# Performance work log

Hardware: AMD Instinct MI355X
Metric: run time of the kernel (lower is better)

## Reference

```python
import jax, jax.numpy as jnp
import numpy as np
from jax import lax

NUM_CLASSES = 102
IN_CAPS = 2592
IN_DIM = 8
OUT_DIM = 16
ROUTINGS = 3
IMG = 112

def squash(s, axis=-1, eps=1e-8):
    sq = jnp.sum(s * s, axis=axis, keepdims=True)
    return (sq / (1.0 + sq)) * s / jnp.sqrt(sq + eps)

def conv2d(x, w, b, stride):
    y = lax.conv_general_dilated(x, w, (stride, stride), 'VALID',
                                 dimension_numbers=('NCHW', 'OIHW', 'NCHW'))
    return y + b[None, :, None, None]

def setup_inputs() -> dict:
    key = jax.random.key(0)
    ks = jax.random.split(key, 12)
    B = 32
    x = jax.random.normal(ks[0], (B, 3, IMG, IMG), jnp.float32)
    targets = jax.random.randint(ks[1], (B,), 0, NUM_CLASSES)
    conv1_w = jax.random.normal(ks[2], (256, 3, 11, 11), jnp.float32) * 0.02
    conv1_b = jnp.zeros((256,), jnp.float32)
    pc_w = jax.random.normal(ks[3], (256, 256, 9, 9), jnp.float32) * 0.02
    pc_b = jnp.zeros((256,), jnp.float32)
    W = jax.random.normal(ks[4], (NUM_CLASSES, IN_CAPS, OUT_DIM, IN_DIM), jnp.float32) * 0.01
    fc1_w = jax.random.normal(ks[5], (NUM_CLASSES * OUT_DIM, 512), jnp.float32) * 0.02
    fc1_b = jnp.zeros((512,), jnp.float32)
    fc2_w = jax.random.normal(ks[6], (512, 1024), jnp.float32) * 0.02
    fc2_b = jnp.zeros((1024,), jnp.float32)
    fc3_w = jax.random.normal(ks[7], (1024, 3 * IMG * IMG), jnp.float32) * 0.02
    fc3_b = jnp.zeros((3 * IMG * IMG,), jnp.float32)
    return dict(x=x, targets=targets, conv1_w=conv1_w, conv1_b=conv1_b,
                pc_w=pc_w, pc_b=pc_b, W=W,
                fc1_w=fc1_w, fc1_b=fc1_b, fc2_w=fc2_w, fc2_b=fc2_b,
                fc3_w=fc3_w, fc3_b=fc3_b)

def reference(x, targets, conv1_w, conv1_b, pc_w, pc_b, W,
              fc1_w, fc1_b, fc2_w, fc2_b, fc3_w, fc3_b):
    B = x.shape[0]
    # conv backbone: [B,3,112,112] -> [B,256,34,34]
    feat = jax.nn.relu(conv2d(x, conv1_w, conv1_b, 3))
    # primary caps conv: -> [B,256,9,9] -> [B,2592,8], squash
    pc = conv2d(feat, pc_w, pc_b, 3)
    u = squash(pc.reshape(B, IN_CAPS, IN_DIM))
    # prediction vectors: [B, O, N, D_out]
    x_hat = jnp.einsum('ondi,bni->bond', W, u)
    x_hat_sg = lax.stop_gradient(x_hat)
    b = jnp.zeros((B, NUM_CLASSES, IN_CAPS), x.dtype)
    v = None
    for it in range(ROUTINGS):
        c = jax.nn.softmax(b, axis=1)  # couple over out caps
        xh = x_hat if it == ROUTINGS - 1 else x_hat_sg
        s = jnp.einsum('bon,bond->bod', c, xh)
        v = squash(s)
        if it < ROUTINGS - 1:
            b = b + jnp.einsum('bond,bod->bon', xh, v)
    # reconstruction: mask by target class capsule
    mask = jax.nn.one_hot(targets, NUM_CLASSES, dtype=v.dtype)
    h = (v * mask[:, :, None]).reshape(B, NUM_CLASSES * OUT_DIM)
    h = jax.nn.relu(h @ fc1_w + fc1_b)
    h = jax.nn.relu(h @ fc2_w + fc2_b)
    recon = jax.nn.sigmoid(h @ fc3_w + fc3_b).reshape(B, 3, IMG, IMG)
    return (v, recon)
```

## Files before the change

### kernel.cpp

```cpp
#include <hip/hip_runtime.h>
#include <hip/hip_fp16.h>
#include <math.h>

#define B32   32
#define OCLS  102
#define NCAPS 2592

#define OFF_FEAT   0u
#define OFF_WQ2    0u
#define OFF_C1WT   10027008u
#define OFF_PCWQ   10119936u
#define OFF_PCP    15428352u
#define OFF_WQ     15428352u
#define OFF_U2     26045184u
#define OFF_CT     26708736u
#define OFF_FC3P   26045184u
#define OFF_S      30938880u
#define OFF_V0     30991104u
#define OFF_V1     31043328u
#define OFF_VSQ    31095552u
#define OFF_H1     31108608u
#define OFF_H2T    31124992u

typedef __attribute__((ext_vector_type(8))) short short8;
typedef __attribute__((ext_vector_type(4))) float f32x4;
typedef long long i64;

__device__ __forceinline__ unsigned short f2b(float f) {
  union { float f; unsigned u; } v; v.f = f;
  unsigned r = v.u + 0x7fffu + ((v.u >> 16) & 1u);
  return (unsigned short)(r >> 16);
}

__device__ __forceinline__ unsigned f2q_fast(float x) {
  union { float f; unsigned u; } v; v.f = x;
  unsigned s = (v.u >> 24) & 0x80u;
  unsigned au = v.u & 0x7fffffffu;
  if (au < 0x3c800000u) return s;
  if (au >= 0x43e00000u) return s | 0x7eu;
  unsigned r = au + 0x7ffffu + ((au >> 20) & 1u);
  unsigned e = (r >> 23) - 120u;
  unsigned m = (r >> 20) & 7u;
  return s | (e << 3) | m;
}

__device__ __forceinline__ unsigned fp8pair(float a, float b) {
#if __has_builtin(__builtin_amdgcn_cvt_pk_fp8_f32)
  return (unsigned)__builtin_amdgcn_cvt_pk_fp8_f32(a, b, 0, false) & 0xffffu;
#else
  return f2q_fast(a) | (f2q_fast(b) << 8);
#endif
}

__global__ void k_mkC1B(const float* __restrict__ conv1_w,
                        unsigned short* __restrict__ C1WB) {
  int co = blockIdx.x;
  int t = threadIdx.x;
#pragma unroll
  for (int ci = 0; ci < 3; ++ci) {
    float v = (t < 121) ? conv1_w[co * 363 + ci * 121 + t] : 0.f;
    C1WB[(ci * 256 + co) * 128 + t] = f2b(v);
  }
}

__global__ void k_mkBq(const float* __restrict__ pc_w, unsigned char* __restrict__ PCWQ) {
  int co = blockIdx.x;
  for (int e = threadIdx.x; e < 20736; e += 256) {
    int ci = e / 81, tap = e - ci * 81;
    PCWQ[(size_t)ci * 26624 + co * 104 + tap] =
        (unsigned char)f2q_fast(pc_w[(size_t)co * 20736 + e] * 64.f);
  }
  int ci = threadIdx.x;
  for (int tap = 81; tap < 104; ++tap)
    PCWQ[(size_t)ci * 26624 + co * 104 + tap] = 0;
}

__global__ __launch_bounds__(256) void k_mkW2(const float* __restrict__ W,
                                              unsigned char* __restrict__ Wq2,
                                              unsigned char* __restrict__ Wq) {
  __shared__ unsigned char sq[32 * 128];
  int t = threadIdx.x;
  size_t base = (size_t)blockIdx.x * 4096;
  const float4* src = (const float4*)(W + base + (size_t)t * 16);
  float4 f0 = src[0], f1 = src[1], f2 = src[2], f3 = src[3];
  float v[16] = {f0.x, f0.y, f0.z, f0.w, f1.x, f1.y, f1.z, f1.w,
                 f2.x, f2.y, f2.z, f2.w, f3.x, f3.y, f3.z, f3.w};
  unsigned words[4];
#pragma unroll
  for (int j = 0; j < 4; ++j)
    words[j] = fp8pair(v[4 * j] * 64.f, v[4 * j + 1] * 64.f) |
               (fp8pair(v[4 * j + 2] * 64.f, v[4 * j + 3] * 64.f) << 16);
  *(uint4*)(Wq2 + base + (size_t)t * 16) =
      make_uint4(words[0], words[1], words[2], words[3]);

  int r = t >> 3, seg = t & 7;
#pragma unroll
  for (int e = 0; e < 16; ++e) {
    unsigned byte = (words[e >> 2] >> ((e & 3) * 8)) & 0xffu;
    int idx = seg * 16 + e, d = idx >> 3, i = idx & 7;
    sq[r * 128 + i * 16 + d] = (unsigned char)byte;
  }
  __syncthreads();
  *(uint4*)(Wq + base + (size_t)t * 16) = ((const uint4*)sq)[t];
}

__global__ __launch_bounds__(256) void k_c1m(const float* __restrict__ x,
                                             const unsigned short* __restrict__ C1WB,
                                             const float* __restrict__ bias,
                                             float* __restrict__ feat2) {
  __shared__ unsigned short sh[48 * 128 + 128 * 128];
  unsigned short* lA = sh;
  unsigned short* lB = sh + 48 * 128;
  float* obuf = (float*)(sh + 48 * 128);

  int bx = blockIdx.x;
  int hf = blockIdx.y;
  int b = bx / 34, ho = bx % 34;
  int t = threadIdx.x;
  int lane = t & 63, wv = t >> 6;
  int l15 = lane & 15, lh = lane >> 4;
  int rx = l15 & 7;

  {
    uint4 zz = make_uint4(0, 0, 0, 0);
    uint4* z = (uint4*)lA;
    for (int i = t; i < 48 * 128 / 8; i += 256) z[i] = zz;
  }
  __syncthreads();

  f32x4 acc[3][2];
#pragma unroll
  for (int mf = 0; mf < 3; ++mf)
#pragma unroll
    for (int nf = 0; nf < 2; ++nf) acc[mf][nf] = (f32x4){0.f, 0.f, 0.f, 0.f};

#pragma unroll 1
  for (int ci = 0; ci < 3; ++ci) {
    {
      const uint4* Bsrc = (const uint4*)(C1WB + ci * 32768 + hf * 16384);
#pragma unroll
      for (int i = 0; i < 8; ++i) {
        int f = i * 256 + t;
        int row = f >> 4, cu = f & 15;
        ((uint4*)lB)[row * 16 + (cu ^ (row & 7))] = Bsrc[f];
      }
    }
    for (int tk = t; tk < 374; tk += 256) {
      int kh = tk / 34, wo = tk - kh * 34;
      const float* src = x + ((size_t)(b * 3 + ci) * 112 + ho * 3 + kh) * 112 + wo * 3;
#pragma unroll
      for (int j = 0; j < 11; ++j) {
        int tap = kh * 11 + j;
        int cu = tap >> 3;
        lA[wo * 128 + (((cu ^ (wo & 7)) << 3) | (tap & 7))] = f2b(src[j]);
      }
    }
    __syncthreads();

#pragma unroll
    for (int s = 0; s < 4; ++s) {
      int cub = ((s * 4 + lh) ^ rx) << 3;
      short8 a0 = *(const short8*)(lA + (0 + l15) * 128 + cub);
      short8 a1 = *(const short8*)(lA + (16 + l15) * 128 + cub);
      short8 a2 = *(const short8*)(lA + (32 + l15) * 128 + cub);
      short8 b0 = *(const short8*)(lB + (wv * 32 + 0 + l15) * 128 + cub);
      short8 b1 = *(const short8*)(lB + (wv * 32 + 16 + l15) * 128 + cub);
      acc[0][0] = __builtin_amdgcn_mfma_f32_16x16x32_bf16(a0, b0, acc[0][0], 0, 0, 0);
      acc[0][1] = __builtin_amdgcn_mfma_f32_16x16x32_bf16(a0, b1, acc[0][1], 0, 0, 0);
      acc[1][0] = __builtin_amdgcn_mfma_f32_16x16x32_bf16(a1, b0, acc[1][0], 0, 0, 0);
      acc[1][1] = __builtin_amdgcn_mfma_f32_16x16x32_bf16(a1, b1, acc[1][1], 0, 0, 0);
      acc[2][0] = __builtin_amdgcn_mfma_f32_16x16x32_bf16(a2, b0, acc[2][0], 0, 0, 0);
      acc[2][1] = __builtin_amdgcn_mfma_f32_16x16x32_bf16(a2, b1, acc[2][1], 0, 0, 0);
    }
    __syncthreads();
  }

  float bv[2];
#pragma unroll
  for (int nf = 0; nf < 2; ++nf) bv[nf] = bias[hf * 128 + wv * 32 + nf * 16 + l15];
#pragma unroll
  for (int mf = 0; mf < 3; ++mf)
#pragma unroll
    for (int nf = 0; nf < 2; ++nf)
#pragma unroll
      for (int r = 0; r < 4; ++r) {
        int wo = mf * 16 + lh * 4 + r;
        if (wo < 36)
          obuf[(wv * 32 + nf * 16 + l15) * 36 + wo] = fmaxf(acc[mf][nf][r] + bv[nf], 0.f);
      }
  __syncthreads();
  float4* dst = (float4*)(feat2 + (size_t)bx * 9216 + hf * 4608);
  const float4* srcb = (const float4*)obuf;
  for (int i = t; i < 1152; i += 256) dst[i] = srcb[i];
}

__device__ __forceinline__ void pc_gather8(const float* __restrict__ feat2,
                                           unsigned char* __restrict__ dstbuf,
                                           int mb, int ci, int t) {
  for (int task = t; task < 576; task += 256) {
    int m = task / 9, kh = task - m * 9;
    int gm = mb * 64 + m;
    if (gm < 2592) {
      int b = gm / 81, p = gm - b * 81;
      int ho = p / 9, wo = p - ho * 9;
      const float* src = feat2 + ((size_t)(b * 34 + ho * 3 + kh) * 256 + ci) * 36 + wo * 3;
      unsigned char* dst = dstbuf + m * 104 + kh * 9;
      unsigned p01 = fp8pair(src[0], src[1]);
      unsigned p23 = fp8pair(src[2], src[3]);
      unsigned p45 = fp8pair(src[4], src[5]);
      unsigned p67 = fp8pair(src[6], src[7]);
      unsigned p8  = fp8pair(src[8], 0.f);
      dst[0] = p01; dst[1] = p01 >> 8;
      dst[2] = p23; dst[3] = p23 >> 8;
      dst[4] = p45; dst[5] = p45 >> 8;
      dst[6] = p67; dst[7] = p67 >> 8;
      dst[8] = p8;
    }
  }
}

__global__ __launch_bounds__(256, 3) void k_pc4(const float* __restrict__ feat2,
                                                const unsigned char* __restrict__ PCWQ,
                                                __half* __restrict__ pcp) {
  __shared__ unsigned char lA[2][64 * 104];

  int mb = blockIdx.x, kc = blockIdx.y;
  int t = threadIdx.x;
  int lane = t & 63, wv = t >> 6;
  int l15 = lane & 15, lh = lane >> 4;

  {
    uint4 zz = make_uint4(0, 0, 0, 0);
    uint4* z = (uint4*)lA;
    for (int i = t; i < 2 * 64 * 104 / 16; i += 256) z[i] = zz;
  }
  __syncthreads();
  pc_gather8(feat2, lA[0], mb, kc * 8, t);
  __syncthreads();

  f32x4 acc[4][4];
#pragma unroll
  for (int mf = 0; mf < 4; ++mf)
#pragma unroll
    for (int nf = 0; nf < 4; ++nf) acc[mf][nf] = (f32x4){0.f, 0.f, 0.f, 0.f};

#pragma unroll 1
  for (int cil = 0; cil < 8; ++cil) {
    int ci = kc * 8 + cil;
    int cur = cil & 1;

    i64 bfr[4][3];
    const unsigned char* Bbase = PCWQ + (size_t)ci * 26624 + (wv * 64 + l15) * 104 + lh * 8;
#pragma unroll
    for (int nf = 0; nf < 4; ++nf)
#pragma unroll
      for (int s = 0; s < 3; ++s)
        bfr[nf][s] = *(const i64*)(Bbase + nf * 16 * 104 + s * 32);

    if (cil < 7) pc_gather8(feat2, lA[cur ^ 1], mb, ci + 1, t);

    const unsigned char* arow = lA[cur] + l15 * 104 + lh * 8;
#pragma unroll
    for (int s = 0; s < 3; ++s) {
      i64 a0 = *(const i64*)(arow + s * 32);
      i64 a1 = *(const i64*)(arow + 16 * 104 + s * 32);
      i64 a2 = *(const i64*)(arow + 32 * 104 + s * 32);
      i64 a3 = *(const i64*)(arow + 48 * 104 + s * 32);
      acc[0][0] = __builtin_amdgcn_mfma_f32_16x16x32_fp8_fp8(a0, bfr[0][s], acc[0][0], 0, 0, 0);
      acc[0][1] = __builtin_amdgcn_mfma_f32_16x16x32_fp8_fp8(a0, bfr[1][s], acc[0][1], 0, 0, 0);
      acc[0][2] = __builtin_amdgcn_mfma_f32_16x16x32_fp8_fp8(a0, bfr[2][s], acc[0][2], 0, 0, 0);
      acc[0][3] = __builtin_amdgcn_mfma_f32_16x16x32_fp8_fp8(a0, bfr[3][s], acc[0][3], 0, 0, 0);
      acc[1][0] = __builtin_amdgcn_mfma_f32_16x16x32_fp8_fp8(a1, bfr[0][s], acc[1][0], 0, 0, 0);
      acc[1][1] = __builtin_amdgcn_mfma_f32_16x16x32_fp8_fp8(a1, bfr[1][s], acc[1][1], 0, 0, 0);
      acc[1][2] = __builtin_amdgcn_mfma_f32_16x16x32_fp8_fp8(a1, bfr[2][s], acc[1][2], 0, 0, 0);
      acc[1][3] = __builtin_amdgcn_mfma_f32_16x16x32_fp8_fp8(a1, bfr[3][s], acc[1][3], 0, 0, 0);
      acc[2][0] = __builtin_amdgcn_mfma_f32_16x16x32_fp8_fp8(a2, bfr[0][s], acc[2][0], 0, 0, 0);
      acc[2][1] = __builtin_amdgcn_mfma_f32_16x16x32_fp8_fp8(a2, bfr[1][s], acc[2][1], 0, 0, 0);
      acc[2][2] = __builtin_amdgcn_mfma_f32_16x16x32_fp8_fp8(a2, bfr[2][s], acc[2][2], 0, 0, 0);
      acc[2][3] = __builtin_amdgcn_mfma_f32_16x16x32_fp8_fp8(a2, bfr[3][s], acc[2][3], 0, 0, 0);
      acc[3][0] = __builtin_amdgcn_mfma_f32_16x16x32_fp8_fp8(a3, bfr[0][s], acc[3][0], 0, 0, 0);
      acc[3][1] = __builtin_amdgcn_mfma_f32_16x16x32_fp8_fp8(a3, bfr[1][s], acc[3][1], 0, 0, 0);
      acc[3][2] = __builtin_amdgcn_mfma_f32_16x16x32_fp8_fp8(a3, bfr[2][s], acc[3][2], 0, 0, 0);
      acc[3][3] = __builtin_amdgcn_mfma_f32_16x16x32_fp8_fp8(a3, bfr[3][s], acc[3][3], 0, 0, 0);
    }
    __syncthreads();
  }

#pragma unroll
  for (int mf = 0; mf < 4; ++mf) {
    int gm = mb * 64 + mf * 16 + lh * 4;
    if (gm < 2592) {
      __half* dst = pcp + (size_t)kc * 663552 + (size_t)gm * 256 + wv * 64 + l15;
#pragma unroll
      for (int nf = 0; nf < 4; ++nf)
#pragma unroll
        for (int r = 0; r < 4; ++r)
          dst[(size_t)r * 256 + nf * 16] = __float2half(acc[mf][nf][r]);
    }
  }
}

__global__ __launch_bounds__(256) void k_rs(const __half* __restrict__ pcp,
                                            const float* __restrict__ pcb,
                                            float* __restrict__ u2) {
  __shared__ float tile[81 * 17];
  int b = blockIdx.x;
  int cog = blockIdx.y;
  int c0 = cog * 16;
  int t = threadIdx.x;

  for (int e = t; e < 1296; e += 256) {
    int p = e >> 4, col = e & 15;
    const __half* base = pcp + (size_t)(b * 81 + p) * 256 + c0 + col;
    float s = 0.f;
#pragma unroll
    for (int c = 0; c < 32; ++c) s += __half2float(base[(size_t)c * 663552]);
    tile[p * 17 + col] = pcb[c0 + col] + s * 0.015625f;
  }
  __syncthreads();

  if (t < 162) {
    float v[8];
    float sq = 0.f;
#pragma unroll
    for (int i = 0; i < 8; ++i) {
      int g = t * 8 + i;
      int col = g / 81, p = g - col * 81;
      v[i] = tile[p * 17 + col];
      sq += v[i] * v[i];
    }
    float sc = (sq / (1.f + sq)) / sqrtf(sq + 1e-8f);
    int n = cog * 162 + t;
    float4* dst = (float4*)(u2 + ((size_t)b * 2592 + n) * 8);
    dst[0] = make_float4(v[0] * sc, v[1] * sc, v[2] * sc, v[3] * sc);
    dst[1] = make_float4(v[4] * sc, v[5] * sc, v[6] * sc, v[7] * sc);
  }
}

__global__ __launch_bounds__(128) void k_A2(const unsigned char* __restrict__ Wq,
                                            const float* __restrict__ u2,
                                            const unsigned char* __restrict__ vq,
                                            __half* __restrict__ cT) {
  __shared__ __half Eld[102 * 2 * 2 * 32];
  int nb = blockIdx.x;
  int t = threadIdx.x, wv = t >> 6, lane = t & 63;
  int l15 = lane & 15, g = lane >> 4;
  int n0 = nb * 4 + 2 * wv;
  int nl = g >> 1, ih = (g & 1) * 4;

  float4 u0 = *(const float4*)(u2 + (((size_t)l15 * 2592 + n0 + nl) * 8 + ih));
  float4 u1 = *(const float4*)(u2 + (((size_t)(l15 + 16) * 2592 + n0 + nl) * 8 + ih));

  int nlA = l15 >> 3, iA = l15 & 7;
  const unsigned char* Ap = Wq + (((size_t)(n0 + nlA)) * 8 + iA) * 16 + (g & 1) * 8;
  const unsigned char* B0p = vq + (size_t)l15 * 16 + (g & 1) * 8;
  bool act = (g < 2);

  float den0 = 0.f, den1 = 0.f;
#pragma unroll 2
  for (int o = 0; o < 102; ++o) {
    i64 a = 0, b0 = 0, b1 = 0;
    if (act) {
      a  = *(const i64*)(Ap + (size_t)o * 331776);
      b0 = *(const i64*)(B0p + (size_t)o * 512);
      b1 = *(const i64*)(B0p + (size_t)o * 512 + 256);
    }
    f32x4 d0 = {0.f, 0.f, 0.f, 0.f}, d1 = {0.f, 0.f, 0.f, 0.f};
    d0 = __builtin_amdgcn_mfma_f32_16x16x32_fp8_fp8(a, b0, d0, 0, 0, 0);
    d1 = __builtin_amdgcn_mfma_f32_16x16x32_fp8_fp8(a, b1, d1, 0, 0, 0);
    float p0 = d0[0] * u0.x + d0[1] * u0.y + d0[2] * u0.z + d0[3] * u0.w;
    float p1 = d1[0] * u1.x + d1[1] * u1.y + d1[2] * u1.z + d1[3] * u1.w;
    p0 += __shfl_xor(p0, 16);
    p1 += __shfl_xor(p1, 16);
    p0 *= 1.52587890625e-05f;
    p1 *= 1.52587890625e-05f;
    float e0 = __expf(p0), e1 = __expf(p1);
    den0 += e0; den1 += e1;
    if ((g & 1) == 0) {
      int base = (o * 2 + wv) * 64 + (g >> 1) * 16 + l15;
      Eld[base] = __float2half(e0);
      Eld[base + 32] = __float2half(e1);
    }
  }
  float r0 = 1.0f / den0, r1 = 1.0f / den1;
  if ((g & 1) == 0) {
    for (int o = 0; o < 102; ++o) {
      int base = (o * 2 + wv) * 64 + (g >> 1) * 16 + l15;
      float c0 = __half2float(Eld[base]) * r0;
      float c1 = __half2float(Eld[base + 32]) * r1;
      __half* dst = cT + ((size_t)o * 2592 + n0 + (g >> 1)) * 32 + l15;
      dst[0] = __float2half(c0);
      dst[16] = __float2half(c1);
    }
  }
}

__device__ __forceinline__ i64 cu_pack8(float c, float4 a, float4 b) {
  union { unsigned u[2]; i64 v; } r;
  r.u[0] = fp8pair(c * a.x, c * a.y) | (fp8pair(c * a.z, c * a.w) << 16);
  r.u[1] = fp8pair(c * b.x, c * b.y) | (fp8pair(c * b.z, c * b.w) << 16);
  return r.v;
}

template <bool HASC>
__global__ __launch_bounds__(256) void k_B3(const unsigned char* __restrict__ Wq2,
                                            const float* __restrict__ u2,
                                            const __half* __restrict__ cT,
                                            float* __restrict__ s) {
  int o = blockIdx.x, kc = blockIdx.y;
  int t = threadIdx.x, lane = t & 63, wv = t >> 6;
  int l15 = lane & 15, h = lane >> 4;

  f32x4 acc0 = {0.f, 0.f, 0.f, 0.f}, acc1 = {0.f, 0.f, 0.f, 0.f};

#pragma unroll 1
  for (int st = wv; st < 54; st += 4) {
    int n = kc * 216 + st * 4 + h;
    i64 aq = *(const i64*)(Wq2 + (((size_t)o * 2592 + n) * 16 + l15) * 8);

    const float4* u0p = (const float4*)(u2 + ((size_t)l15 * 2592 + n) * 8);
    float4 u0a = u0p[0], u0b = u0p[1];
    const float4* u1p = (const float4*)(u2 + ((size_t)(l15 + 16) * 2592 + n) * 8);
    float4 u1a = u1p[0], u1b = u1p[1];

    float c0 = 16.0f, c1 = 16.0f;
    if (HASC) {
      const __half* cp = cT + ((size_t)o * 2592 + n) * 32;
      c0 = 16.0f * __half2float(cp[l15]);
      c1 = 16.0f * __half2float(cp[l15 + 16]);
    }
    i64 b0 = cu_pack8(c0, u0a, u0b);
    i64 b1 = cu_pack8(c1, u1a, u1b);

    acc0 = __builtin_amdgcn_mfma_f32_16x16x32_fp8_fp8(aq, b0, acc0, 0, 0, 0);
    acc1 = __builtin_amdgcn_mfma_f32_16x16x32_fp8_fp8(aq, b1, acc1, 0, 0, 0);
  }

#pragma unroll
  for (int r = 0; r < 4; ++r) {
    atomicAdd(s + ((size_t)l15 * 102 + o) * 16 + h * 4 + r, acc0[r]);
    atomicAdd(s + ((size_t)(l15 + 16) * 102 + o) * 16 + h * 4 + r, acc1[r]);
  }
}

__global__ void k_R(const float* __restrict__ s, float scale,
                    float* __restrict__ vout, const float* __restrict__ addin,
                    unsigned char* __restrict__ vsq, float* __restrict__ szero) {
  int t = blockIdx.x * 256 + threadIdx.x;
  if (t >= 3264) return;
  const float* sp = s + t * 16;
  float r[16];
  float sq = 0.f;
#pragma unroll
  for (int d = 0; d < 16; ++d) {
    r[d] = sp[d] * scale;
    sq += r[d] * r[d];
  }
  if (szero) {
#pragma unroll
    for (int d = 0; d < 16; ++d) szero[t * 16 + d] = 0.f;
  }
  float sc = (sq / (1.f + sq)) / sqrtf(sq + 1e-8f);
  float vv[16];
#pragma unroll
  for (int d = 0; d < 16; ++d) {
    vv[d] = r[d] * sc;
    vout[t * 16 + d] = vv[d];
  }
  if (vsq) {
    int b = t / 102, o = t - b * 102;
    float w[16];
#pragma unroll
    for (int d = 0; d < 16; ++d)
      w[d] = (addin ? (addin[t * 16 + d] + vv[d]) : vv[d]) * 1024.f;
    unsigned words[4];
#pragma unroll
    for (int q = 0; q < 4; ++q)
      words[q] = fp8pair(w[4 * q], w[4 * q + 1]) | (fp8pair(w[4 * q + 2], w[4 * q + 3]) << 16);
    *(uint4*)(vsq + ((size_t)o * 32 + b) * 16) =
        make_uint4(words[0], words[1], words[2], words[3]);
  }
}

__global__ void k_fc1(const float* __restrict__ v2, const int* __restrict__ tgt,
                      const float* __restrict__ w1, const float* __restrict__ b1,
                      float* __restrict__ h1) {
  int j = blockIdx.x * 128 + threadIdx.x;
  int bq = blockIdx.y;
#pragma unroll
  for (int bi = 0; bi < 4; ++bi) {
    int b = bq * 4 + bi;
    int tb = tgt[b];
    float acc = b1[j];
    const float* vv = v2 + (b * 102 + tb) * 16;
    const float* wr = w1 + (tb * 16) * 512 + j;
#pragma unroll
    for (int d = 0; d < 16; ++d) acc += vv[d] * wr[d * 512];
    h1[b * 512 + j] = fmaxf(acc, 0.f);
  }
}

__global__ void k_fc2(const float* __restrict__ h1, const float* __restrict__ w2,
                      const float* __restrict__ b2, float* __restrict__ h2T) {
  int j = blockIdx.x * 128 + threadIdx.x;
  int bq = blockIdx.y;
  float acc[4];
#pragma unroll
  for (int bi = 0; bi < 4; ++bi) acc[bi] = b2[j];
  for (int k = 0; k < 512; ++k) {
    float wv = w2[k * 1024 + j];
#pragma unroll
    for (int bi = 0; bi < 4; ++bi) acc[bi] += h1[(bq * 4 + bi) * 512 + k] * wv;
  }
  float4 o;
  o.x = fmaxf(acc[0], 0.f); o.y = fmaxf(acc[1], 0.f);
  o.z = fmaxf(acc[2], 0.f); o.w = fmaxf(acc[3], 0.f);
  *(float4*)(h2T + j * 32 + bq * 4) = o;
}

__global__ void k_fc3a(const float* __restrict__ h2T, const float* __restrict__ w3,
                       float* __restrict__ p) {
  int j = blockIdx.x * 128 + threadIdx.x;
  int ky = blockIdx.y;
  float acc[32];
#pragma unroll
  for (int i = 0; i < 32; ++i) acc[i] = 0.f;
  int k0 = ky * 256;
  for (int k = k0; k < k0 + 256; ++k) {
    float wv = w3[(size_t)k * 37632 + j];
    const float4* hp = (const float4*)(h2T + k * 32);
#pragma unroll
    for (int q = 0; q < 8; ++q) {
      float4 h = hp[q];
      acc[q * 4 + 0] += h.x * wv; acc[q * 4 + 1] += h.y * wv;
      acc[q * 4 + 2] += h.z * wv; acc[q * 4 + 3] += h.w * wv;
    }
  }
#pragma unroll
  for (int i = 0; i < 32; ++i)
    p[((size_t)ky * 32 + i) * 37632 + j] = acc[i];
}

__global__ void k_fc3b(const float* __restrict__ p, const float* __restrict__ b3,
                       float* __restrict__ out) {
  int j = blockIdx.x * 256 + threadIdx.x;
  float bv = b3[j];
#pragma unroll 1
  for (int b = 0; b < 32; ++b) {
    float s = bv + p[(size_t)b * 37632 + j] + p[(size_t)(32 + b) * 37632 + j] +
              p[(size_t)(64 + b) * 37632 + j] + p[(size_t)(96 + b) * 37632 + j];
    out[52224 + (size_t)b * 37632 + j] = 1.0f / (1.0f + __expf(-s));
  }
}

extern "C" void kernel_launch(void* const* d_in, const int* in_sizes, int n_in,
                              void* d_out, int out_size, void* d_ws, size_t ws_size,
                              hipStream_t stream) {
  const float* x       = (const float*)d_in[0];
  const int*   targets = (const int*)d_in[1];
  const float* conv1_w = (const float*)d_in[2];
  const float* conv1_b = (const float*)d_in[3];
  const float* pc_w    = (const float*)d_in[4];
  const float* pc_b    = (const float*)d_in[5];
  const float* W       = (const float*)d_in[6];
  const float* fc1_w   = (const float*)d_in[7];
  const float* fc1_b   = (const float*)d_in[8];
  const float* fc2_w   = (const float*)d_in[9];
  const float* fc2_b   = (const float*)d_in[10];
  const float* fc3_w   = (const float*)d_in[11];
  const float* fc3_b   = (const float*)d_in[12];
  float* out = (float*)d_out;
  float* ws = (float*)d_ws;

  float* FEAT2 = ws + OFF_FEAT;
  unsigned short* C1WB = (unsigned short*)(ws + OFF_C1WT);
  unsigned char* PCWQ = (unsigned char*)(ws + OFF_PCWQ);
  __half* PCP = (__half*)(ws + OFF_PCP);
  float* U2   = ws + OFF_U2;
  unsigned char* WQ2 = (unsigned char*)(ws + OFF_WQ2);
  unsigned char* WQ  = (unsigned char*)(ws + OFF_WQ);
  __half* CT  = (__half*)(ws + OFF_CT);
  float* FC3P = ws + OFF_FC3P;
  float* S    = ws + OFF_S;
  float* V0   = ws + OFF_V0;
  float* V1   = ws + OFF_V1;
  unsigned char* VSQ = (unsigned char*)(ws + OFF_VSQ);
  float* H1   = ws + OFF_H1;
  float* H2T  = ws + OFF_H2T;

  k_mkC1B<<<dim3(256), 128, 0, stream>>>(conv1_w, C1WB);
  k_mkBq<<<dim3(256), 256, 0, stream>>>(pc_w, PCWQ);

  k_c1m<<<dim3(1088, 2), 256, 0, stream>>>(x, C1WB, conv1_b, FEAT2);

  k_pc4<<<dim3(41, 32), 256, 0, stream>>>(FEAT2, PCWQ, PCP);
  k_rs<<<dim3(32, 16), 256, 0, stream>>>(PCP, pc_b, U2);

  k_mkW2<<<dim3(8262), 256, 0, stream>>>(W, WQ2, WQ);

  hipMemsetAsync(S, 0, 52224 * sizeof(float), stream);
  k_B3<false><<<dim3(102, 12), 256, 0, stream>>>(WQ2, U2, nullptr, S);
  k_R<<<dim3(13), 256, 0, stream>>>(S, 1.0f / (102.0f * 1024.0f), V0, nullptr, VSQ, S);

  k_A2<<<dim3(648), 128, 0, stream>>>(WQ, U2, VSQ, CT);
  k_B3<true><<<dim3(102, 12), 256, 0, stream>>>(WQ2, U2, CT, S);
  k_R<<<dim3(13), 256, 0, stream>>>(S, 1.0f / 1024.0f, V1, V0, VSQ, S);

  k_A2<<<dim3(648), 128, 0, stream>>>(WQ, U2, VSQ, CT);
  k_B3<true><<<dim3(102, 12), 256, 0, stream>>>(WQ2, U2, CT, S);
  k_R<<<dim3(13), 256, 0, stream>>>(S, 1.0f / 1024.0f, out, nullptr, nullptr, nullptr);

  k_fc1<<<dim3(4, 8), 128, 0, stream>>>(out, targets, fc1_w, fc1_b, H1);
  k_fc2<<<dim3(8, 8), 128, 0, stream>>>(H1, fc2_w, fc2_b, H2T);
  k_fc3a<<<dim3(294, 4), 128, 0, stream>>>(H2T, fc3_w, FC3P);
  k_fc3b<<<dim3(147), 256, 0, stream>>>(FC3P, fc3_b, out);
}
```

Before: 636.0 us.

## Merge weight-packing kernels, halve pc split-K, split softmax kernel over class chunks

Three packing kernels become one launch, and the workspace is re-laid out so the buffers no longer alias. The primary-caps conv split-K drops from 32 to 16 chunks, so the reduction kernel reads half as many partials while each block does twice the work. The coupling kernel is split three ways over output classes and writes unnormalised exponentials straight to global memory. It accumulates the softmax denominators atomically, and k_B3 now divides by them, with k_R zeroing the denominator buffer. This trades fewer launches and more parallelism in the routing step for extra atomics and extra global reads.

```diff
diff --git a/kernel.cpp b/kernel.cpp
--- a/kernel.cpp
+++ b/kernel.cpp
@@ -7,20 +7,21 @@
 #define NCAPS 2592
 
 #define OFF_FEAT   0u
-#define OFF_WQ2    0u
 #define OFF_C1WT   10027008u
-#define OFF_PCWQ   10119936u
-#define OFF_PCP    15428352u
-#define OFF_WQ     15428352u
-#define OFF_U2     26045184u
-#define OFF_CT     26708736u
-#define OFF_FC3P   26045184u
-#define OFF_S      30938880u
-#define OFF_V0     30991104u
-#define OFF_V1     31043328u
-#define OFF_VSQ    31095552u
-#define OFF_H1     31108608u
-#define OFF_H2T    31124992u
+#define OFF_PCWQ   10076160u
+#define OFF_PCP    11780096u
+#define OFF_WQ2    17088512u
+#define OFF_WQ     25555456u
+#define OFF_U2     34022400u
+#define OFF_CT     34685952u
+#define OFF_DEN    38916096u
+#define OFF_S      38999040u
+#define OFF_V0     39051264u
+#define OFF_V1     39103488u
+#define OFF_VSQ    39155712u
+#define OFF_H1     39168768u
+#define OFF_H2T    39185152u
+#define OFF_FC3P   39217920u
 
 typedef __attribute__((ext_vector_type(8))) short short8;
 typedef __attribute__((ext_vector_type(4))) float f32x4;
@@ -52,56 +53,64 @@
 #endif
 }
 
-__global__ void k_mkC1B(const float* __restrict__ conv1_w,
-                        unsigned short* __restrict__ C1WB) {
-  int co = blockIdx.x;
-  int t = threadIdx.x;
-#pragma unroll
-  for (int ci = 0; ci < 3; ++ci) {
-    float v = (t < 121) ? conv1_w[co * 363 + ci * 121 + t] : 0.f;
-    C1WB[(ci * 256 + co) * 128 + t] = f2b(v);
-  }
-}
-
-__global__ void k_mkBq(const float* __restrict__ pc_w, unsigned char* __restrict__ PCWQ) {
-  int co = blockIdx.x;
-  for (int e = threadIdx.x; e < 20736; e += 256) {
-    int ci = e / 81, tap = e - ci * 81;
-    PCWQ[(size_t)ci * 26624 + co * 104 + tap] =
-        (unsigned char)f2q_fast(pc_w[(size_t)co * 20736 + e] * 64.f);
-  }
-  int ci = threadIdx.x;
-  for (int tap = 81; tap < 104; ++tap)
-    PCWQ[(size_t)ci * 26624 + co * 104 + tap] = 0;
-}
-
-__global__ __launch_bounds__(256) void k_mkW2(const float* __restrict__ W,
+__device__ __forceinline__ float rcpf(float x) {
+#if __has_builtin(__builtin_amdgcn_rcpf)
+  return __builtin_amdgcn_rcpf(x);
+#else
+  return 1.0f / x;
+#endif
+}
+
+__global__ __launch_bounds__(256) void k_pack(const float* __restrict__ conv1_w,
+                                              const float* __restrict__ pc_w,
+                                              const float* __restrict__ W,
+                                              unsigned short* __restrict__ C1WB,
+                                              unsigned char* __restrict__ PCWQ,
                                               unsigned char* __restrict__ Wq2,
                                               unsigned char* __restrict__ Wq) {
   __shared__ unsigned char sq[32 * 128];
+  int bb = blockIdx.x;
   int t = threadIdx.x;
-  size_t base = (size_t)blockIdx.x * 4096;
-  const float4* src = (const float4*)(W + base + (size_t)t * 16);
-  float4 f0 = src[0], f1 = src[1], f2 = src[2], f3 = src[3];
-  float v[16] = {f0.x, f0.y, f0.z, f0.w, f1.x, f1.y, f1.z, f1.w,
-                 f2.x, f2.y, f2.z, f2.w, f3.x, f3.y, f3.z, f3.w};
-  unsigned words[4];
-#pragma unroll
-  for (int j = 0; j < 4; ++j)
-    words[j] = fp8pair(v[4 * j] * 64.f, v[4 * j + 1] * 64.f) |
-               (fp8pair(v[4 * j + 2] * 64.f, v[4 * j + 3] * 64.f) << 16);
-  *(uint4*)(Wq2 + base + (size_t)t * 16) =
-      make_uint4(words[0], words[1], words[2], words[3]);
-
-  int r = t >> 3, seg = t & 7;
-#pragma unroll
-  for (int e = 0; e < 16; ++e) {
-    unsigned byte = (words[e >> 2] >> ((e & 3) * 8)) & 0xffu;
-    int idx = seg * 16 + e, d = idx >> 3, i = idx & 7;
-    sq[r * 128 + i * 16 + d] = (unsigned char)byte;
-  }
-  __syncthreads();
-  *(uint4*)(Wq + base + (size_t)t * 16) = ((const uint4*)sq)[t];
+  if (bb < 256) {
+    if (t < 128) {
+#pragma unroll
+      for (int ci = 0; ci < 3; ++ci) {
+        float v = (t < 121) ? conv1_w[bb * 363 + ci * 121 + t] : 0.f;
+        C1WB[(ci * 256 + bb) * 128 + t] = f2b(v);
+      }
+    }
+  } else if (bb < 512) {
+    int co = bb - 256;
+    for (int e = t; e < 20736; e += 256) {
+      int ci = e / 81, tap = e - ci * 81;
+      PCWQ[(size_t)ci * 26624 + co * 104 + tap] =
+          (unsigned char)f2q_fast(pc_w[(size_t)co * 20736 + e] * 64.f);
+    }
+    for (int tap = 81; tap < 104; ++tap)
+      PCWQ[(size_t)t * 26624 + co * 104 + tap] = 0;
+  } else {
+    size_t base = (size_t)(bb - 512) * 4096;
+    const float4* src = (const float4*)(W + base + (size_t)t * 16);
+    float4 f0 = src[0], f1 = src[1], f2 = src[2], f3 = src[3];
+    float v[16] = {f0.x, f0.y, f0.z, f0.w, f1.x, f1.y, f1.z, f1.w,
+                   f2.x, f2.y, f2.z, f2.w, f3.x, f3.y, f3.z, f3.w};
+    unsigned words[4];
+#pragma unroll
+    for (int j = 0; j < 4; ++j)
+      words[j] = fp8pair(v[4 * j] * 64.f, v[4 * j + 1] * 64.f) |
+                 (fp8pair(v[4 * j + 2] * 64.f, v[4 * j + 3] * 64.f) << 16);
+    *(uint4*)(Wq2 + base + (size_t)t * 16) =
+        make_uint4(words[0], words[1], words[2], words[3]);
+    int r = t >> 3, seg = t & 7;
+#pragma unroll
+    for (int e = 0; e < 16; ++e) {
+      unsigned byte = (words[e >> 2] >> ((e & 3) * 8)) & 0xffu;
+      int idx = seg * 16 + e, d = idx >> 3, i = idx & 7;
+      sq[r * 128 + i * 16 + d] = (unsigned char)byte;
+    }
+    __syncthreads();
+    *(uint4*)(Wq + base + (size_t)t * 16) = ((const uint4*)sq)[t];
+  }
 }
 
 __global__ __launch_bounds__(256) void k_c1m(const float* __restrict__ x,
@@ -235,7 +244,7 @@
     for (int i = t; i < 2 * 64 * 104 / 16; i += 256) z[i] = zz;
   }
   __syncthreads();
-  pc_gather8(feat2, lA[0], mb, kc * 8, t);
+  pc_gather8(feat2, lA[0], mb, kc * 16, t);
   __syncthreads();
 
   f32x4 acc[4][4];
@@ -245,8 +254,8 @@
     for (int nf = 0; nf < 4; ++nf) acc[mf][nf] = (f32x4){0.f, 0.f, 0.f, 0.f};
 
 #pragma unroll 1
-  for (int cil = 0; cil < 8; ++cil) {
-    int ci = kc * 8 + cil;
+  for (int cil = 0; cil < 16; ++cil) {
+    int ci = kc * 16 + cil;
     int cur = cil & 1;
 
     i64 bfr[4][3];
@@ -257,7 +266,7 @@
       for (int s = 0; s < 3; ++s)
         bfr[nf][s] = *(const i64*)(Bbase + nf * 16 * 104 + s * 32);
 
-    if (cil < 7) pc_gather8(feat2, lA[cur ^ 1], mb, ci + 1, t);
+    if (cil < 15) pc_gather8(feat2, lA[cur ^ 1], mb, ci + 1, t);
 
     const unsigned char* arow = lA[cur] + l15 * 104 + lh * 8;
 #pragma unroll
@@ -314,7 +323,7 @@
     const __half* base = pcp + (size_t)(b * 81 + p) * 256 + c0 + col;
     float s = 0.f;
 #pragma unroll
-    for (int c = 0; c < 32; ++c) s += __half2float(base[(size_t)c * 663552]);
+    for (int c = 0; c < 16; ++c) s += __half2float(base[(size_t)c * 663552]);
     tile[p * 17 + col] = pcb[c0 + col] + s * 0.015625f;
   }
   __syncthreads();
@@ -337,12 +346,14 @@
   }
 }
 
-__global__ __launch_bounds__(128) void k_A2(const unsigned char* __restrict__ Wq,
+__global__ __launch_bounds__(128) void k_A3(const unsigned char* __restrict__ Wq,
                                             const float* __restrict__ u2,
                                             const unsigned char* __restrict__ vq,
-                                            __half* __restrict__ cT) {
-  __shared__ __half Eld[102 * 2 * 2 * 32];
+                                            __half* __restrict__ cT,
+                                            float* __restrict__ den) {
   int nb = blockIdx.x;
+  int ch = blockIdx.y;
+  int o0 = ch * 34;
   int t = threadIdx.x, wv = t >> 6, lane = t & 63;
   int l15 = lane & 15, g = lane >> 4;
   int n0 = nb * 4 + 2 * wv;
@@ -352,18 +363,19 @@
   float4 u1 = *(const float4*)(u2 + (((size_t)(l15 + 16) * 2592 + n0 + nl) * 8 + ih));
 
   int nlA = l15 >> 3, iA = l15 & 7;
-  const unsigned char* Ap = Wq + (((size_t)(n0 + nlA)) * 8 + iA) * 16 + (g & 1) * 8;
-  const unsigned char* B0p = vq + (size_t)l15 * 16 + (g & 1) * 8;
+  const unsigned char* Ap = Wq + (((size_t)(n0 + nlA)) * 8 + iA) * 16 + (g & 1) * 8 +
+                            (size_t)o0 * 331776;
+  const unsigned char* B0p = vq + (size_t)l15 * 16 + (g & 1) * 8 + (size_t)o0 * 512;
   bool act = (g < 2);
 
   float den0 = 0.f, den1 = 0.f;
 #pragma unroll 2
-  for (int o = 0; o < 102; ++o) {
+  for (int oo = 0; oo < 34; ++oo) {
     i64 a = 0, b0 = 0, b1 = 0;
     if (act) {
-      a  = *(const i64*)(Ap + (size_t)o * 331776);
-      b0 = *(const i64*)(B0p + (size_t)o * 512);
-      b1 = *(const i64*)(B0p + (size_t)o * 512 + 256);
+      a  = *(const i64*)(Ap + (size_t)oo * 331776);
+      b0 = *(const i64*)(B0p + (size_t)oo * 512);
+      b1 = *(const i64*)(B0p + (size_t)oo * 512 + 256);
     }
     f32x4 d0 = {0.f, 0.f, 0.f, 0.f}, d1 = {0.f, 0.f, 0.f, 0.f};
     d0 = __builtin_amdgcn_mfma_f32_16x16x32_fp8_fp8(a, b0, d0, 0, 0, 0);
@@ -377,21 +389,14 @@
     float e0 = __expf(p0), e1 = __expf(p1);
     den0 += e0; den1 += e1;
     if ((g & 1) == 0) {
-      int base = (o * 2 + wv) * 64 + (g >> 1) * 16 + l15;
-      Eld[base] = __float2half(e0);
-      Eld[base + 32] = __float2half(e1);
-    }
-  }
-  float r0 = 1.0f / den0, r1 = 1.0f / den1;
+      __half* dst = cT + ((size_t)(o0 + oo) * 2592 + n0 + nl) * 32 + l15;
+      dst[0]  = __float2half(e0);
+      dst[16] = __float2half(e1);
+    }
+  }
   if ((g & 1) == 0) {
-    for (int o = 0; o < 102; ++o) {
-      int base = (o * 2 + wv) * 64 + (g >> 1) * 16 + l15;
-      float c0 = __half2float(Eld[base]) * r0;
-      float c1 = __half2float(Eld[base + 32]) * r1;
-      __half* dst = cT + ((size_t)o * 2592 + n0 + (g >> 1)) * 32 + l15;
-      dst[0] = __float2half(c0);
-      dst[16] = __float2half(c1);
-    }
+    atomicAdd(den + (n0 + nl) * 32 + l15, den0);
+    atomicAdd(den + (n0 + nl) * 32 + l15 + 16, den1);
   }
 }
 
@@ -406,6 +411,7 @@
 __global__ __launch_bounds__(256) void k_B3(const unsigned char* __restrict__ Wq2,
                                             const float* __restrict__ u2,
                                             const __half* __restrict__ cT,
+                                            const float* __restrict__ den,
                                             float* __restrict__ s) {
   int o = blockIdx.x, kc = blockIdx.y;
   int t = threadIdx.x, lane = t & 63, wv = t >> 6;
@@ -426,8 +432,10 @@
     float c0 = 16.0f, c1 = 16.0f;
     if (HASC) {
       const __half* cp = cT + ((size_t)o * 2592 + n) * 32;
-      c0 = 16.0f * __half2float(cp[l15]);
-      c1 = 16.0f * __half2float(cp[l15 + 16]);
+      float i0 = rcpf(den[n * 32 + l15]);
+      float i1 = rcpf(den[n * 32 + l15 + 16]);
+      c0 = 16.0f * __half2float(cp[l15]) * i0;
+      c1 = 16.0f * __half2float(cp[l15 + 16]) * i1;
     }
     i64 b0 = cu_pack8(c0, u0a, u0b);
     i64 b1 = cu_pack8(c1, u1a, u1b);
@@ -445,8 +453,12 @@
 
 __global__ void k_R(const float* __restrict__ s, float scale,
                     float* __restrict__ vout, const float* __restrict__ addin,
-                    unsigned char* __restrict__ vsq, float* __restrict__ szero) {
+                    unsigned char* __restrict__ vsq, float* __restrict__ szero,
+                    float* __restrict__ dzero) {
   int t = blockIdx.x * 256 + threadIdx.x;
+  if (dzero) {
+    for (int i = t; i < 82944; i += 3328) dzero[i] = 0.f;
+  }
   if (t >= 3264) return;
   const float* sp = s + t * 16;
   float r[16];
@@ -576,39 +588,37 @@
   unsigned short* C1WB = (unsigned short*)(ws + OFF_C1WT);
   unsigned char* PCWQ = (unsigned char*)(ws + OFF_PCWQ);
   __half* PCP = (__half*)(ws + OFF_PCP);
-  float* U2   = ws + OFF_U2;
   unsigned char* WQ2 = (unsigned char*)(ws + OFF_WQ2);
   unsigned char* WQ  = (unsigned char*)(ws + OFF_WQ);
+  float* U2   = ws + OFF_U2;
   __half* CT  = (__half*)(ws + OFF_CT);
-  float* FC3P = ws + OFF_FC3P;
+  float* DEN  = ws + OFF_DEN;
   float* S    = ws + OFF_S;
   float* V0   = ws + OFF_V0;
   float* V1   = ws + OFF_V1;
   unsigned char* VSQ = (unsigned char*)(ws + OFF_VSQ);
   float* H1   = ws + OFF_H1;
   float* H2T  = ws + OFF_H2T;
-
-  k_mkC1B<<<dim3(256), 128, 0, stream>>>(conv1_w, C1WB);
-  k_mkBq<<<dim3(256), 256, 0, stream>>>(pc_w, PCWQ);
+  float* FC3P = ws + OFF_FC3P;
+
+  k_pack<<<dim3(8774), 256, 0, stream>>>(conv1_w, pc_w, W, C1WB, PCWQ, WQ2, WQ);
 
   k_c1m<<<dim3(1088, 2), 256, 0, stream>>>(x, C1WB, conv1_b, FEAT2);
 
-  k_pc4<<<dim3(41, 32), 256, 0, stream>>>(FEAT2, PCWQ, PCP);
+  k_pc4<<<dim3(41, 16), 256, 0, stream>>>(FEAT2, PCWQ, PCP);
   k_rs<<<dim3(32, 16), 256, 0, stream>>>(PCP, pc_b, U2);
 
-  k_mkW2<<<dim3(8262), 256, 0, stream>>>(W, WQ2, WQ);
-
   hipMemsetAsync(S, 0, 52224 * sizeof(float), stream);
-  k_B3<false><<<dim3(102, 12), 256, 0, stream>>>(WQ2, U2, nullptr, S);
-  k_R<<<dim3(13), 256, 0, stream>>>(S, 1.0f / (102.0f * 1024.0f), V0, nullptr, VSQ, S);
-
-  k_A2<<<dim3(648), 128, 0, stream>>>(WQ, U2, VSQ, CT);
-  k_B3<true><<<dim3(102, 12), 256, 0, stream>>>(WQ2, U2, CT, S);
-  k_R<<<dim3(13), 256, 0, stream>>>(S, 1.0f / 1024.0f, V1, V0, VSQ, S);
-
-  k_A2<<<dim3(648), 128, 0, stream>>>(WQ, U2, VSQ, CT);
-  k_B3<true><<<dim3(102, 12), 256, 0, stream>>>(WQ2, U2, CT, S);
-  k_R<<<dim3(13), 256, 0, stream>>>(S, 1.0f / 1024.0f, out, nullptr, nullptr, nullptr);
+  k_B3<false><<<dim3(102, 12), 256, 0, stream>>>(WQ2, U2, nullptr, nullptr, S);
+  k_R<<<dim3(13), 256, 0, stream>>>(S, 1.0f / (102.0f * 1024.0f), V0, nullptr, VSQ, S, DEN);
+
+  k_A3<<<dim3(648, 3), 128, 0, stream>>>(WQ, U2, VSQ, CT, DEN);
+  k_B3<true><<<dim3(102, 12), 256, 0, stream>>>(WQ2, U2, CT, DEN, S);
+  k_R<<<dim3(13), 256, 0, stream>>>(S, 1.0f / 1024.0f, V1, V0, VSQ, S, DEN);
+
+  k_A3<<<dim3(648, 3), 128, 0, stream>>>(WQ, U2, VSQ, CT, DEN);
+  k_B3<true><<<dim3(102, 12), 256, 0, stream>>>(WQ2, U2, CT, DEN, S);
+  k_R<<<dim3(13), 256, 0, stream>>>(S, 1.0f / 1024.0f, out, nullptr, nullptr, nullptr, nullptr);
 
   k_fc1<<<dim3(4, 8), 128, 0, stream>>>(out, targets, fc1_w, fc1_b, H1);
   k_fc2<<<dim3(8, 8), 128, 0, stream>>>(H1, fc2_w, fc2_b, H2T);
```

Measured after the change: 549.4 us. 1.16x faster.
